# Performance work log

Hardware: AMD Instinct MI355X
Metric: run time of the kernel (lower is better)

The kernel has to match this reference:

```python
import jax, jax.numpy as jnp
import numpy as np

N = 100000          # nodes
E = 1600000         # edges (avg degree 16)
D_IN = 128
D_OUT = 128
K = 3               # Chebyshev order
LAMBDA_MAX = 2.0    # PyG default for sym normalization


def setup_inputs() -> dict:
    key = jax.random.key(0)
    k1, k2, k3, k4 = jax.random.split(key, 4)
    x = jax.random.normal(k1, (N, D_IN), dtype=jnp.float32)
    edge_index = jax.random.randint(k2, (2, E), 0, N, dtype=jnp.int32)
    # Glorot-ish init for the K per-order linear weights
    weight = jax.random.normal(k3, (K, D_IN, D_OUT), dtype=jnp.float32) * (1.0 / np.sqrt(D_IN))
    bias = jax.random.normal(k4, (D_OUT,), dtype=jnp.float32) * 0.01
    return {"x": x, "edge_index": edge_index, "weight": weight, "bias": bias}


def reference(x, edge_index, weight, bias):
    src, dst = edge_index[0], edge_index[1]
    n = x.shape[0]

    # remove self loops (zero their weight), symmetric normalization
    ew = jnp.where(src != dst, 1.0, 0.0).astype(x.dtype)
    deg = jax.ops.segment_sum(ew, src, num_segments=n)
    dis = jnp.where(deg > 0, jax.lax.rsqrt(jnp.maximum(deg, 1.0)), 0.0)
    norm = dis[src] * ew * dis[dst]          # D^-1/2 A D^-1/2 entries

    # scaled Laplacian T-hat = (2/lmax) L - I, L = I - A_norm
    off_w = -(2.0 / LAMBDA_MAX) * norm       # off-diagonal entries
    diag_w = 2.0 / LAMBDA_MAX - 1.0          # = 0 for lambda_max=2

    def spmm(h):  # T-hat @ h : gather-multiply-scatter over edges
        agg = jax.ops.segment_sum(off_w[:, None] * h[src], dst, num_segments=n)
        return agg + diag_w * h

    # Chebyshev recurrence: Tx_k = 2 T-hat Tx_{k-1} - Tx_{k-2}
    Tx0 = x
    out = Tx0 @ weight[0]
    Tx1 = spmm(Tx0)
    out = out + Tx1 @ weight[1]
    for k in range(2, weight.shape[0]):
        Tx2 = 2.0 * spmm(Tx1) - Tx0
        out = out + Tx2 @ weight[k]
        Tx0, Tx1 = Tx1, Tx2
    return out + bias
```

## Files before the change

kernel.cpp:

```cpp
#include <hip/hip_runtime.h>
#include <hip/hip_bf16.h>

typedef __hip_bfloat16 bf16;
typedef __attribute__((ext_vector_type(8))) short short8;
typedef __attribute__((ext_vector_type(4))) float float4v;

#define N_NODES 100000
#define M_PAD   100096
#define N_EDGES 1600000
#define D 128
#define K_CAT 384
#define BUCKET_CAP 64
#define NBIN 392
#define BIN_CAP 4608
#define CHUNK 4096

__device__ __forceinline__ float b2f(bf16 v) { return __bfloat162float(v); }
__device__ __forceinline__ bf16 f2b(float v) { return __float2bfloat16(v); }
__device__ __forceinline__ float us2f(unsigned short u) {
    unsigned int x = ((unsigned int)u) << 16;
    return __uint_as_float(x);
}

__global__ void prep_w_kernel(const float* __restrict__ w, const float* __restrict__ bias,
                              bf16* __restrict__ wT, float* __restrict__ biasf) {
    int i = blockIdx.x * blockDim.x + threadIdx.x;
    if (i < D * K_CAT) {
        int o = i / K_CAT, k = i % K_CAT;
        float v;
        if (k < 128) {
            v = w[k * D + o] - w[2 * 16384 + k * D + o];
        } else if (k < 256) {
            v = w[16384 + (k - 128) * D + o];
        } else {
            v = 2.0f * w[2 * 16384 + (k - 256) * D + o];
        }
        wT[i] = f2b(v);
    }
    if (i < D) biasf[i] = bias[i];
}

__global__ __launch_bounds__(256) void convx_kernel(const float* __restrict__ x,
                                                    bf16* __restrict__ xb) {
    int i = (blockIdx.x * 256 + threadIdx.x) * 4;
    float4 v = *(const float4*)(x + i);
    unsigned int p0 = (unsigned int)__bfloat16_as_ushort(f2b(v.x)) |
                      ((unsigned int)__bfloat16_as_ushort(f2b(v.y)) << 16);
    unsigned int p1 = (unsigned int)__bfloat16_as_ushort(f2b(v.z)) |
                      ((unsigned int)__bfloat16_as_ushort(f2b(v.w)) << 16);
    uint2 pk; pk.x = p0; pk.y = p1;
    *(uint2*)(xb + i) = pk;
}

__global__ __launch_bounds__(256) void phaseA_kernel(const int* __restrict__ src,
                                                     const int* __restrict__ dst,
                                                     int* __restrict__ gCursD,
                                                     int* __restrict__ gCursS,
                                                     unsigned int* __restrict__ gBinD,
                                                     unsigned char* __restrict__ gBinS) {
    __shared__ int histD[NBIN], histS[NBIN], cursD[NBIN], cursS[NBIN];
    int tid = threadIdx.x;
    for (int t = tid; t < NBIN; t += 256) { histD[t] = 0; histS[t] = 0; }
    __syncthreads();
    int e0 = blockIdx.x * CHUNK;
    for (int i = tid; i < CHUNK; i += 256) {
        int e = e0 + i;
        if (e >= N_EDGES) break;
        int s = src[e], d = dst[e];
        if (s == d) continue;
        atomicAdd(&histD[d >> 8], 1);
        atomicAdd(&histS[s >> 8], 1);
    }
    __syncthreads();
    for (int t = tid; t < NBIN; t += 256) {
        cursD[t] = (histD[t] > 0) ? atomicAdd(&gCursD[t], histD[t]) : 0;
        cursS[t] = (histS[t] > 0) ? atomicAdd(&gCursS[t], histS[t]) : 0;
    }
    __syncthreads();
    for (int i = tid; i < CHUNK; i += 256) {
        int e = e0 + i;
        if (e >= N_EDGES) break;
        int s = src[e], d = dst[e];
        if (s == d) continue;
        int bd = d >> 8, bs = s >> 8;
        int sd = atomicAdd(&cursD[bd], 1);
        if (sd < BIN_CAP) gBinD[(size_t)bd * BIN_CAP + sd] = ((unsigned int)s << 8) | (unsigned int)(d & 255);
        int ss = atomicAdd(&cursS[bs], 1);
        if (ss < BIN_CAP) gBinS[(size_t)bs * BIN_CAP + ss] = (unsigned char)(s & 255);
    }
}

__global__ __launch_bounds__(256) void phaseB_kernel(const int* __restrict__ gCursD,
                                                     const int* __restrict__ gCursS,
                                                     const unsigned int* __restrict__ gBinD,
                                                     const unsigned char* __restrict__ gBinS,
                                                     int* __restrict__ cnt,
                                                     float* __restrict__ dis,
                                                     int* __restrict__ bucket) {
    __shared__ int curs[256];
    int tid = threadIdx.x;
    int b = blockIdx.x;
    curs[tid] = 0;
    __syncthreads();
    if (b < NBIN) {
        int count = min(gCursD[b], BIN_CAP);
        const unsigned int* rec = gBinD + (size_t)b * BIN_CAP;
        int n0 = b << 8;
        for (int j = tid; j < count; j += 256) {
            unsigned int r = rec[j];
            int dloc = r & 255;
            int s = (int)(r >> 8);
            int slot = atomicAdd(&curs[dloc], 1);
            if (slot < BUCKET_CAP) bucket[(size_t)(n0 + dloc) * BUCKET_CAP + slot] = s;
        }
        __syncthreads();
        int n = n0 + tid;
        if (n < N_NODES) cnt[n] = curs[tid];
    } else {
        int bb = b - NBIN;
        int count = min(gCursS[bb], BIN_CAP);
        const unsigned char* rec = gBinS + (size_t)bb * BIN_CAP;
        for (int j = tid; j < count; j += 256) {
            atomicAdd(&curs[rec[j]], 1);
        }
        __syncthreads();
        int n = (bb << 8) + tid;
        if (n < N_NODES) {
            int c = curs[tid];
            dis[n] = (c > 0) ? rsqrtf((float)c) : 0.0f;
        }
    }
}

__global__ __launch_bounds__(256) void spmm_kernel(const bf16* __restrict__ h,
                                                   const float* __restrict__ dis,
                                                   const int* __restrict__ cnt,
                                                   const int* __restrict__ bucket,
                                                   bf16* __restrict__ outp) {
    int wv = threadIdx.x >> 6;
    int lane = threadIdx.x & 63;
    int n = blockIdx.x * 4 + wv;
    int c = min(cnt[n], BUCKET_CAP);
    float dn = dis[n];
    int s_l = 0;
    float w_l = 0.0f;
    if (lane < c) {
        s_l = bucket[n * BUCKET_CAP + lane];
        w_l = -dis[s_l] * dn;
    }
    int f0 = lane * 2;
    float ax = 0.0f, ay = 0.0f;
    int j = 0;
    for (; j + 4 <= c; j += 4) {
        int s0 = __shfl(s_l, j + 0), s1 = __shfl(s_l, j + 1);
        int s2 = __shfl(s_l, j + 2), s3 = __shfl(s_l, j + 3);
        float w0 = __shfl(w_l, j + 0), w1 = __shfl(w_l, j + 1);
        float w2 = __shfl(w_l, j + 2), w3 = __shfl(w_l, j + 3);
        unsigned int u0 = *(const unsigned int*)(h + (size_t)s0 * D + f0);
        unsigned int u1 = *(const unsigned int*)(h + (size_t)s1 * D + f0);
        unsigned int u2 = *(const unsigned int*)(h + (size_t)s2 * D + f0);
        unsigned int u3 = *(const unsigned int*)(h + (size_t)s3 * D + f0);
        ax += w0 * us2f((unsigned short)(u0 & 0xffff)) + w1 * us2f((unsigned short)(u1 & 0xffff))
            + w2 * us2f((unsigned short)(u2 & 0xffff)) + w3 * us2f((unsigned short)(u3 & 0xffff));
        ay += w0 * us2f((unsigned short)(u0 >> 16)) + w1 * us2f((unsigned short)(u1 >> 16))
            + w2 * us2f((unsigned short)(u2 >> 16)) + w3 * us2f((unsigned short)(u3 >> 16));
    }
    for (; j < c; j++) {
        int sj = __shfl(s_l, j);
        float wj = __shfl(w_l, j);
        unsigned int u = *(const unsigned int*)(h + (size_t)sj * D + f0);
        ax += wj * us2f((unsigned short)(u & 0xffff));
        ay += wj * us2f((unsigned short)(u >> 16));
    }
    unsigned int pk = (unsigned int)__bfloat16_as_ushort(f2b(ax)) |
                      ((unsigned int)__bfloat16_as_ushort(f2b(ay)) << 16);
    *(unsigned int*)(outp + (size_t)n * D + f0) = pk;
}

#define AS_STRIDE 40
__global__ __launch_bounds__(256) void gemm_kernel(const float* __restrict__ x,
                                                   const bf16* __restrict__ tx1,
                                                   const bf16* __restrict__ agg2,
                                                   const bf16* __restrict__ wT,
                                                   const float* __restrict__ biasf,
                                                   float* __restrict__ out) {
    __shared__ bf16 As[128 * AS_STRIDE];
    __shared__ bf16 Bs[128 * AS_STRIDE];

    int tid = threadIdx.x;
    int nb = blockIdx.x * 128;
    int w = tid >> 6;
    int lane = tid & 63;
    int lq = lane >> 4;
    int lr = lane & 15;

    float4v acc[2][8];
#pragma unroll
    for (int i = 0; i < 2; i++)
#pragma unroll
        for (int j = 0; j < 8; j++) acc[i][j] = (float4v)0.0f;

    for (int kc = 0; kc < 12; kc++) {
        int kbase = kc * 32;
        if (kc < 4) {
#pragma unroll
            for (int t = 0; t < 4; t++) {
                int c = tid + t * 256;
                int row = c >> 3;
                int off = (c & 7) * 4;
                int gr = nb + row;
                if (gr > N_NODES - 1) gr = N_NODES - 1;
                float4 v = *(const float4*)(x + (size_t)gr * D + kbase + off);
                unsigned int p0 = (unsigned int)__bfloat16_as_ushort(f2b(v.x)) |
                                  ((unsigned int)__bfloat16_as_ushort(f2b(v.y)) << 16);
                unsigned int p1 = (unsigned int)__bfloat16_as_ushort(f2b(v.z)) |
                                  ((unsigned int)__bfloat16_as_ushort(f2b(v.w)) << 16);
                uint2 pk; pk.x = p0; pk.y = p1;
                *(uint2*)(As + row * AS_STRIDE + off) = pk;
            }
        } else {
            const bf16* Asrc = (kc < 8) ? tx1 : agg2;
            int soff = (kc & 3) * 32;
#pragma unroll
            for (int t = 0; t < 2; t++) {
                int c = tid + t * 256;
                int row = c >> 2;
                int off = (c & 3) * 8;
                uint4 v = *(const uint4*)(Asrc + (size_t)(nb + row) * D + soff + off);
                *(uint4*)(As + row * AS_STRIDE + off) = v;
            }
        }
#pragma unroll
        for (int t = 0; t < 2; t++) {
            int c = tid + t * 256;
            int row = c >> 2;
            int off = (c & 3) * 8;
            uint4 v = *(const uint4*)(wT + (size_t)row * K_CAT + kbase + off);
            *(uint4*)(Bs + row * AS_STRIDE + off) = v;
        }
        __syncthreads();

        short8 af[2], bfr[8];
#pragma unroll
        for (int i = 0; i < 2; i++)
            af[i] = *(const short8*)(As + (w * 32 + i * 16 + lr) * AS_STRIDE + lq * 8);
#pragma unroll
        for (int j = 0; j < 8; j++)
            bfr[j] = *(const short8*)(Bs + (j * 16 + lr) * AS_STRIDE + lq * 8);
#pragma unroll
        for (int i = 0; i < 2; i++)
#pragma unroll
            for (int j = 0; j < 8; j++)
                acc[i][j] = __builtin_amdgcn_mfma_f32_16x16x32_bf16(af[i], bfr[j], acc[i][j], 0, 0, 0);
        __syncthreads();
    }

#pragma unroll
    for (int i = 0; i < 2; i++) {
        int rowb = nb + w * 32 + i * 16 + lq * 4;
#pragma unroll
        for (int j = 0; j < 8; j++) {
            int col = j * 16 + lr;
            float bv = biasf[col];
#pragma unroll
            for (int r = 0; r < 4; r++) {
                int row = rowb + r;
                if (row < N_NODES) out[(size_t)row * D + col] = acc[i][j][r] + bv;
            }
        }
    }
}

extern "C" void kernel_launch(void* const* d_in, const int* in_sizes, int n_in,
                              void* d_out, int out_size, void* d_ws, size_t ws_size,
                              hipStream_t stream) {
    const float* x    = (const float*)d_in[0];
    const int*   ei   = (const int*)d_in[1];
    const float* w    = (const float*)d_in[2];
    const float* bias = (const float*)d_in[3];
    float* out = (float*)d_out;

    char* p = (char*)d_ws;
    int*   cnt    = (int*)p;            p += (size_t)N_NODES * 4;
    float* dis    = (float*)p;          p += (size_t)N_NODES * 4;
    int*   gCurs  = (int*)p;            p += (size_t)2 * NBIN * 4;
    int*   bucket = (int*)p;            p += (size_t)N_NODES * BUCKET_CAP * 4;
    bf16*  buf1   = (bf16*)p;           p += (size_t)M_PAD * D * 2;
    bf16*  buf2   = (bf16*)p;           p += (size_t)M_PAD * D * 2;
    bf16*  wT     = (bf16*)p;           p += (size_t)D * K_CAT * 2;
    float* biasf  = (float*)p;          p += (size_t)D * 4;

    int*   gCursD = gCurs;
    int*   gCursS = gCurs + NBIN;
    unsigned int*  gBinD = (unsigned int*)buf1;
    unsigned char* gBinS = (unsigned char*)(gBinD + (size_t)NBIN * BIN_CAP);
    bf16* xb   = buf2;
    bf16* tx1  = buf1;
    bf16* agg2 = buf2;

    hipMemsetAsync(gCurs, 0, (size_t)2 * NBIN * 4, stream);

    prep_w_kernel<<<(D * K_CAT + 255) / 256, 256, 0, stream>>>(w, bias, wT, biasf);
    convx_kernel<<<(N_NODES * D) / 1024, 256, 0, stream>>>(x, xb);
    phaseA_kernel<<<(N_EDGES + CHUNK - 1) / CHUNK, 256, 0, stream>>>(ei, ei + N_EDGES,
                                                                     gCursD, gCursS, gBinD, gBinS);
    phaseB_kernel<<<2 * NBIN, 256, 0, stream>>>(gCursD, gCursS, gBinD, gBinS, cnt, dis, bucket);
    spmm_kernel<<<N_NODES / 4, 256, 0, stream>>>(xb, dis, cnt, bucket, tx1);
    spmm_kernel<<<N_NODES / 4, 256, 0, stream>>>(tx1, dis, cnt, bucket, agg2);
    gemm_kernel<<<M_PAD / 128, 256, 0, stream>>>(x, tx1, agg2, wT, biasf, out);
}
```

Before: 366.9 us.

## Split feature matrices into 16-wide slabs for cache-local SpMM gathers

Stores the bf16 node features in eight slabs of 16 features each, laid out node-major within a slab. The SpMM grid is split per slab, with eight lanes per node, so each gather reads a 32-byte row segment from a slab of about 3.2 MB that can stay in cache. The GEMM A-tile loads are changed to read the slab layout. The cost is that bucket indices and dis are re-read once per slab (eight times), and each gather becomes a smaller access.

```diff
diff --git a/kernel.cpp b/kernel.cpp
--- a/kernel.cpp
+++ b/kernel.cpp
@@ -14,6 +14,10 @@
 #define NBIN 392
 #define BIN_CAP 4608
 #define CHUNK 4096
+
+#define NSLAB 8
+#define SLAB_F 16
+#define SLAB_STRIDE ((size_t)M_PAD * SLAB_F)
 
 __device__ __forceinline__ float b2f(bf16 v) { return __bfloat162float(v); }
 __device__ __forceinline__ bf16 f2b(float v) { return __float2bfloat16(v); }
@@ -41,15 +45,17 @@
 }
 
 __global__ __launch_bounds__(256) void convx_kernel(const float* __restrict__ x,
-                                                    bf16* __restrict__ xb) {
+                                                    bf16* __restrict__ xs) {
     int i = (blockIdx.x * 256 + threadIdx.x) * 4;
+    int node = i >> 7;
+    int f = i & 127;
     float4 v = *(const float4*)(x + i);
     unsigned int p0 = (unsigned int)__bfloat16_as_ushort(f2b(v.x)) |
                       ((unsigned int)__bfloat16_as_ushort(f2b(v.y)) << 16);
     unsigned int p1 = (unsigned int)__bfloat16_as_ushort(f2b(v.z)) |
                       ((unsigned int)__bfloat16_as_ushort(f2b(v.w)) << 16);
     uint2 pk; pk.x = p0; pk.y = p1;
-    *(uint2*)(xb + i) = pk;
+    *(uint2*)(xs + (size_t)(f >> 4) * SLAB_STRIDE + (size_t)node * SLAB_F + (f & 15)) = pk;
 }
 
 __global__ __launch_bounds__(256) void phaseA_kernel(const int* __restrict__ src,
@@ -137,44 +143,34 @@
                                                    const int* __restrict__ cnt,
                                                    const int* __restrict__ bucket,
                                                    bf16* __restrict__ outp) {
-    int wv = threadIdx.x >> 6;
-    int lane = threadIdx.x & 63;
-    int n = blockIdx.x * 4 + wv;
+    int b = blockIdx.x;
+    int slab = b & 7;
+    int g = b >> 3;
+    int tid = threadIdx.x;
+    int wv = tid >> 6, lane = tid & 63;
+    int grp = lane >> 3, r = lane & 7;
+    int n = (g << 5) + (wv << 3) + grp;
     int c = min(cnt[n], BUCKET_CAP);
     float dn = dis[n];
-    int s_l = 0;
-    float w_l = 0.0f;
-    if (lane < c) {
-        s_l = bucket[n * BUCKET_CAP + lane];
-        w_l = -dis[s_l] * dn;
-    }
-    int f0 = lane * 2;
+    const bf16* hs = h + (size_t)slab * SLAB_STRIDE;
+    const int* bk = bucket + (size_t)n * BUCKET_CAP;
     float ax = 0.0f, ay = 0.0f;
-    int j = 0;
-    for (; j + 4 <= c; j += 4) {
-        int s0 = __shfl(s_l, j + 0), s1 = __shfl(s_l, j + 1);
-        int s2 = __shfl(s_l, j + 2), s3 = __shfl(s_l, j + 3);
-        float w0 = __shfl(w_l, j + 0), w1 = __shfl(w_l, j + 1);
-        float w2 = __shfl(w_l, j + 2), w3 = __shfl(w_l, j + 3);
-        unsigned int u0 = *(const unsigned int*)(h + (size_t)s0 * D + f0);
-        unsigned int u1 = *(const unsigned int*)(h + (size_t)s1 * D + f0);
-        unsigned int u2 = *(const unsigned int*)(h + (size_t)s2 * D + f0);
-        unsigned int u3 = *(const unsigned int*)(h + (size_t)s3 * D + f0);
-        ax += w0 * us2f((unsigned short)(u0 & 0xffff)) + w1 * us2f((unsigned short)(u1 & 0xffff))
-            + w2 * us2f((unsigned short)(u2 & 0xffff)) + w3 * us2f((unsigned short)(u3 & 0xffff));
-        ay += w0 * us2f((unsigned short)(u0 >> 16)) + w1 * us2f((unsigned short)(u1 >> 16))
-            + w2 * us2f((unsigned short)(u2 >> 16)) + w3 * us2f((unsigned short)(u3 >> 16));
-    }
-    for (; j < c; j++) {
-        int sj = __shfl(s_l, j);
-        float wj = __shfl(w_l, j);
-        unsigned int u = *(const unsigned int*)(h + (size_t)sj * D + f0);
-        ax += wj * us2f((unsigned short)(u & 0xffff));
-        ay += wj * us2f((unsigned short)(u >> 16));
+    for (int j0 = 0; j0 < c; j0 += 8) {
+        int jj = j0 + r;
+        int sl = 0; float wl = 0.0f;
+        if (jj < c) { sl = bk[jj]; wl = -dis[sl] * dn; }
+#pragma unroll
+        for (int u = 0; u < 8; u++) {
+            int sv = __shfl(sl, u, 8);
+            float wu = __shfl(wl, u, 8);
+            unsigned int uv = *(const unsigned int*)(hs + (size_t)sv * SLAB_F + (r << 1));
+            ax += wu * us2f((unsigned short)(uv & 0xffff));
+            ay += wu * us2f((unsigned short)(uv >> 16));
+        }
     }
     unsigned int pk = (unsigned int)__bfloat16_as_ushort(f2b(ax)) |
                       ((unsigned int)__bfloat16_as_ushort(f2b(ay)) << 16);
-    *(unsigned int*)(outp + (size_t)n * D + f0) = pk;
+    *(unsigned int*)(outp + (size_t)slab * SLAB_STRIDE + (size_t)n * SLAB_F + (r << 1)) = pk;
 }
 
 #define AS_STRIDE 40
@@ -226,7 +222,9 @@
                 int c = tid + t * 256;
                 int row = c >> 2;
                 int off = (c & 3) * 8;
-                uint4 v = *(const uint4*)(Asrc + (size_t)(nb + row) * D + soff + off);
+                int f = soff + off;
+                uint4 v = *(const uint4*)(Asrc + (size_t)(f >> 4) * SLAB_STRIDE +
+                                          (size_t)(nb + row) * SLAB_F + (f & 15));
                 *(uint4*)(As + row * AS_STRIDE + off) = v;
             }
         }
@@ -294,18 +292,18 @@
     int*   gCursS = gCurs + NBIN;
     unsigned int*  gBinD = (unsigned int*)buf1;
     unsigned char* gBinS = (unsigned char*)(gBinD + (size_t)NBIN * BIN_CAP);
-    bf16* xb   = buf2;
+    bf16* xs   = buf2;
     bf16* tx1  = buf1;
     bf16* agg2 = buf2;
 
     hipMemsetAsync(gCurs, 0, (size_t)2 * NBIN * 4, stream);
 
     prep_w_kernel<<<(D * K_CAT + 255) / 256, 256, 0, stream>>>(w, bias, wT, biasf);
-    convx_kernel<<<(N_NODES * D) / 1024, 256, 0, stream>>>(x, xb);
+    convx_kernel<<<(N_NODES * D) / 1024, 256, 0, stream>>>(x, xs);
     phaseA_kernel<<<(N_EDGES + CHUNK - 1) / CHUNK, 256, 0, stream>>>(ei, ei + N_EDGES,
                                                                      gCursD, gCursS, gBinD, gBinS);
     phaseB_kernel<<<2 * NBIN, 256, 0, stream>>>(gCursD, gCursS, gBinD, gBinS, cnt, dis, bucket);
-    spmm_kernel<<<N_NODES / 4, 256, 0, stream>>>(xb, dis, cnt, bucket, tx1);
-    spmm_kernel<<<N_NODES / 4, 256, 0, stream>>>(tx1, dis, cnt, bucket, agg2);
+    spmm_kernel<<<NSLAB * (N_NODES / 32), 256, 0, stream>>>(xs, dis, cnt, bucket, tx1);
+    spmm_kernel<<<NSLAB * (N_NODES / 32), 256, 0, stream>>>(tx1, dis, cnt, bucket, agg2);
     gemm_kernel<<<M_PAD / 128, 256, 0, stream>>>(x, tx1, agg2, wT, biasf, out);
 }
```

After: 470.3 us. +28.2%, slower.
